# Optimization experiments

Hardware: AMD Instinct MI355X
Metric: run time of the kernel (lower is better)

Reference implementation:

```python
import jax, jax.numpy as jnp
from jax import lax
import numpy as np

LOD = 60          # latent_obs_dim
LSD = 2 * LOD     # latent state dim
ACT = 10          # action dim
K = 15            # num_basis
BW = 3            # bandwidth
H_CTRL = 60       # control net hidden units
B, T = 1024, 150


def elup1(x):
    # elu(x) + 1, standard RKN positive-variance activation
    return jnp.where(x >= 0, x + 1.0, jnp.exp(x))


def setup_inputs() -> dict:
    key = jax.random.key(0)
    ks = jax.random.split(key, 14)
    inp = {
        "latent_obs": jax.random.normal(ks[0], (B, T, LOD), jnp.float32),
        "obs_vars": jax.random.uniform(ks[1], (B, T, LOD), jnp.float32) + 0.01,
        "action": jax.random.normal(ks[2], (B, T, ACT), jnp.float32),
        "initial_mean": jax.random.normal(ks[3], (B, LSD), jnp.float32),
        "initial_cov_u": jnp.ones((B, LOD), jnp.float32),
        "initial_cov_l": jnp.ones((B, LOD), jnp.float32),
        "initial_cov_s": jnp.zeros((B, LOD), jnp.float32),
        # transition model: K banded basis matrices per quadrant
        "tm11_basis": 0.05 * jax.random.normal(ks[4], (K, LOD, LOD), jnp.float32),
        "tm12_basis": 0.05 * jax.random.normal(ks[5], (K, LOD, LOD), jnp.float32),
        "tm21_basis": 0.05 * jax.random.normal(ks[6], (K, LOD, LOD), jnp.float32),
        "tm22_basis": 0.05 * jax.random.normal(ks[7], (K, LOD, LOD), jnp.float32),
        # coefficient net: linear (no hidden units per default config) + softmax
        "coeff_w": 0.05 * jax.random.normal(ks[8], (LSD, K), jnp.float32),
        "coeff_b": jnp.zeros((K,), jnp.float32),
        # control net: act -> 60 -> ReLU -> lsd
        "ctrl_w1": (1.0 / np.sqrt(ACT)) * jax.random.normal(ks[9], (ACT, H_CTRL), jnp.float32),
        "ctrl_b1": jnp.zeros((H_CTRL,), jnp.float32),
        "ctrl_w2": (1.0 / np.sqrt(H_CTRL)) * jax.random.normal(ks[10], (H_CTRL, LSD), jnp.float32),
        "ctrl_b2": jnp.zeros((LSD,), jnp.float32),
        # learned transition noise (elup1(0) = 1 matches default trans_covar=1)
        "log_trans_cov": jnp.zeros((LSD,), jnp.float32),
    }
    return inp


def _band_mask():
    i = np.arange(LOD)
    return jnp.asarray((np.abs(i[:, None] - i[None, :]) <= BW).astype(np.float32))


def reference(latent_obs, obs_vars, action, initial_mean,
              initial_cov_u, initial_cov_l, initial_cov_s,
              tm11_basis, tm12_basis, tm21_basis, tm22_basis,
              coeff_w, coeff_b, ctrl_w1, ctrl_b1, ctrl_w2, ctrl_b2,
              log_trans_cov):
    mask = _band_mask()
    m11, m12 = tm11_basis * mask, tm12_basis * mask
    m21, m22 = tm21_basis * mask, tm22_basis * mask
    tc = elup1(log_trans_cov)
    tcu, tcl = tc[:LOD], tc[LOD:]

    def mv(tm, v):  # batched matrix-vector: [b,i,j] @ [b,j] -> [b,i]
        return jnp.einsum('bij,bj->bi', tm, v)

    def step(carry, xs):
        mean, cu, cl, cs = carry           # prior belief
        obs, ov, act = xs
        # ---- Update (factorized Kalman update) ----
        denom = cu + ov
        qu = cu / denom                    # upper Kalman gain
        ql = cs / denom                    # lower Kalman gain
        res = obs - mean[:, :LOD]
        post_mean = mean + jnp.concatenate([qu * res, ql * res], axis=-1)
        f = 1.0 - qu
        pcu = f * cu
        pcs = f * cs
        pcl = cl - ql * cs
        # ---- AcPredict (locally linear transition + control) ----
        coeff = jax.nn.softmax(post_mean @ coeff_w + coeff_b, axis=-1)  # [B,K]
        t11 = jnp.einsum('bk,kij->bij', coeff, m11)
        t12 = jnp.einsum('bk,kij->bij', coeff, m12)
        t21 = jnp.einsum('bk,kij->bij', coeff, m21)
        t22 = jnp.einsum('bk,kij->bij', coeff, m22)
        mu, ml = post_mean[:, :LOD], post_mean[:, LOD:]
        ctrl = jax.nn.relu(act @ ctrl_w1 + ctrl_b1) @ ctrl_w2 + ctrl_b2
        nmean = jnp.concatenate([mv(t11, mu) + mv(t12, ml),
                                 mv(t21, mu) + mv(t22, ml)], axis=-1) + ctrl
        # diag blocks of T C T^T with C block-diagonal (cu, cl, cs)
        ncu = mv(t11 ** 2, pcu) + 2.0 * mv(t11 * t12, pcs) + mv(t12 ** 2, pcl) + tcu
        ncl = mv(t21 ** 2, pcu) + 2.0 * mv(t21 * t22, pcs) + mv(t22 ** 2, pcl) + tcl
        ncs = mv(t21 * t11, pcu) + mv(t22 * t11 + t21 * t12, pcs) + mv(t22 * t12, pcl)
        out = (post_mean, pcu, pcl, pcs, nmean, ncu, ncl, ncs)
        return (nmean, ncu, ncl, ncs), out

    xs = (jnp.moveaxis(latent_obs, 1, 0),
          jnp.moveaxis(obs_vars, 1, 0),
          jnp.moveaxis(action, 1, 0))
    carry0 = (initial_mean, initial_cov_u, initial_cov_l, initial_cov_s)
    _, ys = lax.scan(step, carry0, xs)
    post_means, pcu, pcl, pcs, prior_means, ncu, ncl, ncs = [
        jnp.moveaxis(y, 0, 1) for y in ys]  # [B,T,...]
    return (post_means, pcu, pcl, pcs, prior_means, ncu, ncl, ncs)


if __name__ == "__main__":
    outs = reference(**setup_inputs())
    print([o.shape for o in outs])
```

## Files before the change

kernel.cpp:

```cpp
#include <hip/hip_runtime.h>
#include <hip/hip_bf16.h>

namespace {

constexpr int TT = 150;

__device__ __forceinline__ float dot4(float4 a, float4 b) {
  return a.x*b.x + a.y*b.y + a.z*b.z + a.w*b.w;
}
__device__ __forceinline__ unsigned short bf16bits(float v) {
  __hip_bfloat16 h = __float2bfloat16(v);
  return *reinterpret_cast<unsigned short*>(&h);
}
__device__ __forceinline__ float dot2bf(unsigned a, unsigned b, float c) {
  float d;
  asm("v_dot2_f32_bf16 %0, %1, %2, %3" : "=v"(d) : "v"(a), "v"(b), "v"(c));
  return d;
}
__device__ __forceinline__ float tdot(uint4 a, uint4 b, const unsigned* cp) {
  float s = 0.f;
  s = dot2bf(a.x, cp[0], s); s = dot2bf(a.y, cp[1], s);
  s = dot2bf(a.z, cp[2], s); s = dot2bf(a.w, cp[3], s);
  s = dot2bf(b.x, cp[4], s); s = dot2bf(b.y, cp[5], s);
  s = dot2bf(b.z, cp[6], s); s = dot2bf(b.w, cp[7], s);
  return s;
}

template<int D0, int ND>
__device__ __forceinline__ void tmv_part(const uint4* m4u, const unsigned* cepk,
                                         const float* stat, int ii, int b, int swz,
                                         float rv[5]) {
  #pragma unroll
  for (int dd = 0; dd < ND; ++dd) {
    const int d = D0 + dd;
    const int ba = (0*7 + d)*120 + ii*2;
    const int bb = (1*7 + d)*120 + ii*2;
    const int bc = (2*7 + d)*120 + ii*2;
    const int bd = (3*7 + d)*120 + ii*2;
    const uint4 xa = m4u[ba + swz], ya = m4u[ba + 1 - swz];
    const uint4 xb = m4u[bb + swz], yb = m4u[bb + 1 - swz];
    const uint4 xc = m4u[bc + swz], yc = m4u[bc + 1 - swz];
    const uint4 xd = m4u[bd + swz], yd = m4u[bd + 1 - swz];
    const float a11 = tdot(xa, ya, cepk);
    const float a12 = tdot(xb, yb, cepk);
    const float a21 = tdot(xc, yc, cepk);
    const float a22 = tdot(xd, yd, cepk);
    const int si = (ii + d)*4 + b;
    const float mun  = stat[si];
    const float mln  = stat[288  + si];
    const float pcun = stat[576  + si];
    const float pcsn = stat[864  + si];
    const float pcln = stat[1152 + si];
    rv[0] += a11*mun + a12*mln;
    rv[1] += a21*mun + a22*mln;
    rv[2] += a11*a11*pcun + 2.f*a11*a12*pcsn + a12*a12*pcln;
    rv[3] += a21*a21*pcun + 2.f*a21*a22*pcsn + a22*a22*pcln;
    rv[4] += a21*a11*pcun + (a22*a11 + a21*a12)*pcsn + a22*a12*pcln;
  }
}

__launch_bounds__(256, 4)
__global__ void ctrl_pre(const float* __restrict__ actp,
                         const float* __restrict__ w1,
                         const float* __restrict__ b1,
                         const float* __restrict__ w2,
                         const float* __restrict__ b2,
                         float* __restrict__ out)
{
  __shared__ float w1s[640];
  __shared__ float b1s[64];
  __shared__ __align__(16) float w2pk[7680];
  __shared__ float b2s[128];
  __shared__ __align__(16) float hbuf[256];

  const int tid = threadIdx.x;
  for (int idx = tid; idx < 640; idx += 256) {
    const int j = idx & 63, a = idx >> 6;
    w1s[idx] = (j < 60) ? w1[a*60 + j] : 0.f;
  }
  for (int idx = tid; idx < 7680; idx += 256) {
    const int e = idx & 3;
    const int l = (idx >> 2) & 63;
    const int rest = idx >> 8;
    const int j4 = rest % 15;
    const int p  = rest / 15;
    w2pk[idx] = (l < 60) ? w2[(4*j4 + e)*120 + 2*l + p] : 0.f;
  }
  if (tid < 64)  b1s[tid] = (tid < 60)  ? b1[tid] : 0.f;
  if (tid < 128) b2s[tid] = (tid < 120) ? b2[tid] : 0.f;
  __syncthreads();

  const int w = tid >> 6, lane = tid & 63;
  float* o4 = out + 46080000L;
  const float4* w2pk4 = (const float4*)w2pk;
  const float4* hb4   = (const float4*)hbuf;

  long bt = (long)(blockIdx.x*4 + w);
  float av = (lane < 10 && bt < 153600L) ? actp[bt*10 + lane] : 0.f;

  for (int it = 0; it < 10; ++it) {
    const long btn = bt + 16384L;
    const float avn = (lane < 10 && btn < 153600L) ? actp[btn*10 + lane] : 0.f;

    if (bt < 153600L) {
      float hj = b1s[lane];
      #pragma unroll
      for (int a = 0; a < 10; ++a) hj += __shfl(av, a) * w1s[a*64 + lane];
      hbuf[w*64 + lane] = (lane < 60) ? fmaxf(hj, 0.f) : 0.f;

      float s0 = 0.f, s1 = 0.f;
      if (lane < 60) { s0 = b2s[2*lane]; s1 = b2s[2*lane + 1]; }
      #pragma unroll
      for (int j4 = 0; j4 < 15; ++j4) {
        const float4 hq = hb4[w*16 + j4];
        s0 += dot4(hq, w2pk4[(0*15 + j4)*64 + lane]);
        s1 += dot4(hq, w2pk4[(1*15 + j4)*64 + lane]);
      }
      if (lane < 60) ((float2*)(o4 + bt*120))[lane] = make_float2(s0, s1);
    }
    bt = btn; av = avn;
  }
}

__launch_bounds__(1024, 4)
__global__ void acrkn(const float* __restrict__ lob,
                      const float* __restrict__ ovr,
                      const float* __restrict__ im,
                      const float* __restrict__ icu,
                      const float* __restrict__ icl,
                      const float* __restrict__ ics,
                      const float* __restrict__ tm11,
                      const float* __restrict__ tm12,
                      const float* __restrict__ tm21,
                      const float* __restrict__ tm22,
                      const float* __restrict__ cw,
                      const float* __restrict__ cb,
                      const float* __restrict__ ltc,
                      float* __restrict__ out)
{
  __shared__ __align__(16) unsigned m4b[13440];
  __shared__ __align__(16) float cwc[2048];
  __shared__ __align__(16) float stat[1440];
  __shared__ __align__(16) float pscratch[4096];
  __shared__ __align__(16) float parts[256];
  __shared__ __align__(16) float red[5120];
  __shared__ float cbs[16];

  const int tid = threadIdx.x;

  for (int idx = tid; idx < 13440; idx += 1024) {
    const int c2 = idx & 7;
    int rest = idx >> 3;
    const int i = rest % 60;  rest /= 60;
    const int d = rest % 7;
    const int mat = rest / 7;
    const int k0 = 2*c2;
    const int j = i + d - 3;
    const float* tp = (mat == 0) ? tm11 : (mat == 1) ? tm12 : (mat == 2) ? tm21 : tm22;
    float ve = 0.f, vo = 0.f;
    if (j >= 0 && j < 60) {
      ve = tp[(k0*60 + i)*60 + j];
      if (k0 + 1 < 15) vo = tp[((k0+1)*60 + i)*60 + j];
    }
    const unsigned u = ((unsigned)bf16bits(vo) << 16) | (unsigned)bf16bits(ve);
    const int s = c2 >> 2, q = c2 & 3;
    const int sp = s ^ ((i >> 2) & 1);
    m4b[(((mat*7 + d)*60 + i)*2 + sp)*4 + q] = u;
  }
  if (tid < 512) {
    const int f4 = tid;
    const int p = f4 & 127, c = f4 >> 7;
    const int col = (p < 60) ? p : ((p >= 64 && p < 124) ? (p - 4) : -1);
    float v0 = 0.f, v1 = 0.f, v2 = 0.f, v3 = 0.f;
    if (col >= 0) {
      const int k0 = c*4;
      v0 = cw[col*15 + k0+0];
      v1 = cw[col*15 + k0+1];
      v2 = cw[col*15 + k0+2];
      v3 = (k0+3 < 15) ? cw[col*15 + k0+3] : 0.f;
    }
    ((float4*)cwc)[f4] = make_float4(v0, v1, v2, v3);
  }
  for (int idx = tid; idx < 1440; idx += 1024) stat[idx] = 0.f;
  if (tid < 16) cbs[tid] = (tid < 15) ? cb[tid] : 0.f;

  const int w = tid >> 6;
  const int chunk = w >> 2;
  const int wq = w & 3;
  const int lane = tid & 63;
  const int r = lane >> 2;
  const int b = lane & 3;
  const int iraw = wq*16 + r;
  const bool valid = (iraw < 60);
  const int ii = valid ? iraw : 0;
  const int gb = blockIdx.x*4 + b;
  const int swz = (ii >> 2) & 1;

  float mu_c = 0.f, ml_c = 0.f, cu_c = 1.f, cl_c = 1.f, cs_c = 0.f;
  float tcu_r = 1.f, tcl_r = 1.f;
  if (valid) {
    mu_c = im[gb*120 + ii];
    ml_c = im[gb*120 + 60 + ii];
    cu_c = icu[gb*60 + ii];
    cl_c = icl[gb*60 + ii];
    cs_c = ics[gb*60 + ii];
    const float l0 = ltc[ii], l1 = ltc[60 + ii];
    tcu_r = (l0 >= 0.f) ? l0 + 1.f : __expf(l0);
    tcl_r = (l1 >= 0.f) ? l1 + 1.f : __expf(l1);
  }

  const uint4*  m4u    = (const uint4*)m4b;
  const float4* cwc4   = (const float4*)cwc;
  const float4* parts4 = (const float4*)parts;
  float4*       ps4    = (float4*)pscratch;

  float* o0 = out;
  float* o1 = out + 18432000L;
  float* o2 = out + 27648000L;
  float* o3 = out + 36864000L;
  float* o4 = out + 46080000L;
  float* o5 = out + 64512000L;
  float* o6 = out + 73728000L;
  float* o7 = out + 82944000L;

  __syncthreads();

  for (int t = 0; t < TT; ++t) {
    const long ob120 = ((long)gb*TT + t)*120;

    float ctrl_u = 0.f, ctrl_l = 0.f;
    if ((chunk == 0 || chunk == 3) && valid) {
      ctrl_u = o4[ob120 + ii];
      ctrl_l = o4[ob120 + 60 + ii];
    }

    if (chunk == 0) {
      const long ib = (long)gb*(TT*60) + t*60 + ii;
      float obs = 0.f, ovv = 1.f;
      if (valid) { obs = lob[ib]; ovv = ovr[ib]; }
      const float denom = cu_c + ovv;
      const float inv = 1.0f / denom;
      const float qu = cu_c * inv;
      const float ql = cs_c * inv;
      const float res = obs - mu_c;
      float pm_u = mu_c + qu*res;
      float pm_l = ml_c + ql*res;
      const float f1 = 1.f - qu;
      float pcu = f1*cu_c, pcs = f1*cs_c, pcl = cl_c - ql*cs_c;
      if (!valid) { pm_u = 0.f; pm_l = 0.f; pcu = 0.f; pcs = 0.f; pcl = 0.f; }

      if (valid) {
        stat[(0*72 + ii + 3)*4 + b] = pm_u;
        stat[(1*72 + ii + 3)*4 + b] = pm_l;
        stat[(2*72 + ii + 3)*4 + b] = pcu;
        stat[(3*72 + ii + 3)*4 + b] = pcs;
        stat[(4*72 + ii + 3)*4 + b] = pcl;
      }

      float p[16];
      #pragma unroll
      for (int k = 0; k < 16; ++k) p[k] = 0.f;
      #pragma unroll
      for (int c = 0; c < 4; ++c) {
        const float4 wu = cwc4[c*128 + ii];
        const float4 wl = cwc4[c*128 + 64 + ii];
        p[c*4+0] += pm_u*wu.x + pm_l*wl.x;
        p[c*4+1] += pm_u*wu.y + pm_l*wl.y;
        p[c*4+2] += pm_u*wu.z + pm_l*wl.z;
        p[c*4+3] += pm_u*wu.w + pm_l*wl.w;
      }
      const int pb = (wq*64 + lane)*4;
      ps4[pb+0] = make_float4(p[0],  p[1],  p[2],  p[3]);
      ps4[pb+1] = make_float4(p[4],  p[5],  p[6],  p[7]);
      ps4[pb+2] = make_float4(p[8],  p[9],  p[10], p[11]);
      ps4[pb+3] = make_float4(p[12], p[13], p[14], p[15]);
      const int rbase = wq*1024 + b*16 + r;
      float tv[16];
      #pragma unroll
      for (int rp = 0; rp < 16; ++rp) tv[rp] = pscratch[rbase + rp*64];
      const float s0 = (tv[0]+tv[1]) + (tv[2]+tv[3]);
      const float s1 = (tv[4]+tv[5]) + (tv[6]+tv[7]);
      const float s2 = (tv[8]+tv[9]) + (tv[10]+tv[11]);
      const float s3 = (tv[12]+tv[13]) + (tv[14]+tv[15]);
      parts[(wq*4 + b)*16 + r] = (s0+s1) + (s2+s3);
    }
    __syncthreads();

    if (chunk == 3 && valid) {
      const long ob60 = ((long)gb*TT + t)*60;
      const float s_pmu = stat[(0*72 + ii + 3)*4 + b];
      const float s_pml = stat[(1*72 + ii + 3)*4 + b];
      const float s_pcu = stat[(2*72 + ii + 3)*4 + b];
      const float s_pcs = stat[(3*72 + ii + 3)*4 + b];
      const float s_pcl = stat[(4*72 + ii + 3)*4 + b];
      o0[ob120 + ii]      = s_pmu;
      o0[ob120 + 60 + ii] = s_pml;
      o1[ob60 + ii] = s_pcu;
      o2[ob60 + ii] = s_pcl;
      o3[ob60 + ii] = s_pcs;
    }

    float q[16];
    #pragma unroll
    for (int k = 0; k < 16; ++k) q[k] = cbs[k];
    #pragma unroll
    for (int ww = 0; ww < 4; ++ww) {
      #pragma unroll
      for (int c = 0; c < 4; ++c) {
        const float4 pv = parts4[(ww*4 + b)*4 + c];
        q[4*c+0] += pv.x; q[4*c+1] += pv.y; q[4*c+2] += pv.z; q[4*c+3] += pv.w;
      }
    }
    float ce[16];
    #pragma unroll
    for (int k = 0; k < 15; ++k) ce[k] = __expf(q[k]);
    const float e0 = (ce[0]+ce[1]) + (ce[2]+ce[3]);
    const float e1 = (ce[4]+ce[5]) + (ce[6]+ce[7]);
    const float e2 = (ce[8]+ce[9]) + (ce[10]+ce[11]);
    const float e3 = (ce[12]+ce[13]) + ce[14];
    const float rs = 1.f / ((e0+e1) + (e2+e3));
    #pragma unroll
    for (int k = 0; k < 15; ++k) ce[k] *= rs;
    ce[15] = 0.f;
    unsigned cepk[8];
    #pragma unroll
    for (int j = 0; j < 8; ++j)
      cepk[j] = ((unsigned)bf16bits(ce[2*j+1]) << 16) | (unsigned)bf16bits(ce[2*j]);

    float rv[5] = {0.f, 0.f, 0.f, 0.f, 0.f};
    if      (chunk == 0) tmv_part<0, 2>(m4u, cepk, stat, ii, b, swz, rv);
    else if (chunk == 1) tmv_part<2, 2>(m4u, cepk, stat, ii, b, swz, rv);
    else if (chunk == 2) tmv_part<4, 2>(m4u, cepk, stat, ii, b, swz, rv);
    else                 tmv_part<6, 1>(m4u, cepk, stat, ii, b, swz, rv);

    if (valid) {
      #pragma unroll
      for (int v = 0; v < 5; ++v) red[chunk*1280 + v*256 + ii*4 + b] = rv[v];
    }
    __syncthreads();

    if (chunk == 0 || chunk == 3) {
      const int rb = ii*4 + b;
      float nmu = ctrl_u, nml = ctrl_l, ncu = tcu_r, ncl = tcl_r, ncs = 0.f;
      #pragma unroll
      for (int c = 0; c < 4; ++c) {
        nmu += red[c*1280 + 0*256 + rb];
        nml += red[c*1280 + 1*256 + rb];
        ncu += red[c*1280 + 2*256 + rb];
        ncl += red[c*1280 + 3*256 + rb];
        ncs += red[c*1280 + 4*256 + rb];
      }
      if (chunk == 3) {
        if (valid) {
          const long ob60 = ((long)gb*TT + t)*60;
          o4[ob120 + ii]      = nmu;
          o4[ob120 + 60 + ii] = nml;
          o5[ob60 + ii] = ncu;
          o6[ob60 + ii] = ncl;
          o7[ob60 + ii] = ncs;
        }
      } else {
        mu_c = nmu; ml_c = nml; cu_c = ncu; cl_c = ncl; cs_c = ncs;
      }
    }
  }
}

}

extern "C" void kernel_launch(void* const* d_in, const int* in_sizes, int n_in,
                              void* d_out, int out_size, void* d_ws, size_t ws_size,
                              hipStream_t stream) {
  (void)in_sizes; (void)n_in; (void)d_ws; (void)ws_size; (void)out_size;
  const float* lob  = (const float*)d_in[0];
  const float* ovr  = (const float*)d_in[1];
  const float* actp = (const float*)d_in[2];
  const float* im   = (const float*)d_in[3];
  const float* icu  = (const float*)d_in[4];
  const float* icl  = (const float*)d_in[5];
  const float* ics  = (const float*)d_in[6];
  const float* tm11 = (const float*)d_in[7];
  const float* tm12 = (const float*)d_in[8];
  const float* tm21 = (const float*)d_in[9];
  const float* tm22 = (const float*)d_in[10];
  const float* cw   = (const float*)d_in[11];
  const float* cb   = (const float*)d_in[12];
  const float* w1   = (const float*)d_in[13];
  const float* b1   = (const float*)d_in[14];
  const float* w2   = (const float*)d_in[15];
  const float* b2   = (const float*)d_in[16];
  const float* ltc  = (const float*)d_in[17];

  ctrl_pre<<<dim3(4096), dim3(256), 0, stream>>>(actp, w1, b1, w2, b2, (float*)d_out);
  acrkn<<<dim3(256), dim3(1024), 0, stream>>>(
      lob, ovr, im, icu, icl, ics,
      tm11, tm12, tm21, tm22, cw, cb, ltc,
      (float*)d_out);
}
```

Measured before the change: 725.2 us.

## Fuse control net into recurrent kernel using idle wave groups

Removes the separate ctrl_pre kernel and computes the control MLP per timestep inside the main scan kernel on chunks 1 and 2, which were idle during the update phase. The result goes into a double-buffered shared array instead of a global round trip through the prior-mean output. The pscratch reduction layout is also padded (stride 20) to reduce LDS bank conflicts. This adds shared memory (w2T, hctl, ctl) and per-step work on the critical path, which may lower occupancy or lengthen each step.

After: 627.5 us. 13.5% less time.

```diff
diff --git a/kernel.cpp b/kernel.cpp
--- a/kernel.cpp
+++ b/kernel.cpp
@@ -59,72 +59,10 @@
   }
 }
 
-__launch_bounds__(256, 4)
-__global__ void ctrl_pre(const float* __restrict__ actp,
-                         const float* __restrict__ w1,
-                         const float* __restrict__ b1,
-                         const float* __restrict__ w2,
-                         const float* __restrict__ b2,
-                         float* __restrict__ out)
-{
-  __shared__ float w1s[640];
-  __shared__ float b1s[64];
-  __shared__ __align__(16) float w2pk[7680];
-  __shared__ float b2s[128];
-  __shared__ __align__(16) float hbuf[256];
-
-  const int tid = threadIdx.x;
-  for (int idx = tid; idx < 640; idx += 256) {
-    const int j = idx & 63, a = idx >> 6;
-    w1s[idx] = (j < 60) ? w1[a*60 + j] : 0.f;
-  }
-  for (int idx = tid; idx < 7680; idx += 256) {
-    const int e = idx & 3;
-    const int l = (idx >> 2) & 63;
-    const int rest = idx >> 8;
-    const int j4 = rest % 15;
-    const int p  = rest / 15;
-    w2pk[idx] = (l < 60) ? w2[(4*j4 + e)*120 + 2*l + p] : 0.f;
-  }
-  if (tid < 64)  b1s[tid] = (tid < 60)  ? b1[tid] : 0.f;
-  if (tid < 128) b2s[tid] = (tid < 120) ? b2[tid] : 0.f;
-  __syncthreads();
-
-  const int w = tid >> 6, lane = tid & 63;
-  float* o4 = out + 46080000L;
-  const float4* w2pk4 = (const float4*)w2pk;
-  const float4* hb4   = (const float4*)hbuf;
-
-  long bt = (long)(blockIdx.x*4 + w);
-  float av = (lane < 10 && bt < 153600L) ? actp[bt*10 + lane] : 0.f;
-
-  for (int it = 0; it < 10; ++it) {
-    const long btn = bt + 16384L;
-    const float avn = (lane < 10 && btn < 153600L) ? actp[btn*10 + lane] : 0.f;
-
-    if (bt < 153600L) {
-      float hj = b1s[lane];
-      #pragma unroll
-      for (int a = 0; a < 10; ++a) hj += __shfl(av, a) * w1s[a*64 + lane];
-      hbuf[w*64 + lane] = (lane < 60) ? fmaxf(hj, 0.f) : 0.f;
-
-      float s0 = 0.f, s1 = 0.f;
-      if (lane < 60) { s0 = b2s[2*lane]; s1 = b2s[2*lane + 1]; }
-      #pragma unroll
-      for (int j4 = 0; j4 < 15; ++j4) {
-        const float4 hq = hb4[w*16 + j4];
-        s0 += dot4(hq, w2pk4[(0*15 + j4)*64 + lane]);
-        s1 += dot4(hq, w2pk4[(1*15 + j4)*64 + lane]);
-      }
-      if (lane < 60) ((float2*)(o4 + bt*120))[lane] = make_float2(s0, s1);
-    }
-    bt = btn; av = avn;
-  }
-}
-
 __launch_bounds__(1024, 4)
 __global__ void acrkn(const float* __restrict__ lob,
                       const float* __restrict__ ovr,
+                      const float* __restrict__ actp,
                       const float* __restrict__ im,
                       const float* __restrict__ icu,
                       const float* __restrict__ icl,
@@ -135,15 +73,25 @@
                       const float* __restrict__ tm22,
                       const float* __restrict__ cw,
                       const float* __restrict__ cb,
+                      const float* __restrict__ w1,
+                      const float* __restrict__ b1,
+                      const float* __restrict__ w2,
+                      const float* __restrict__ b2,
                       const float* __restrict__ ltc,
                       float* __restrict__ out)
 {
   __shared__ __align__(16) unsigned m4b[13440];
   __shared__ __align__(16) float cwc[2048];
   __shared__ __align__(16) float stat[1440];
-  __shared__ __align__(16) float pscratch[4096];
+  __shared__ __align__(16) float pscratch[5120];
   __shared__ __align__(16) float parts[256];
   __shared__ __align__(16) float red[5120];
+  __shared__ __align__(16) float ctl[1024];
+  __shared__ __align__(16) float hctl[512];
+  __shared__ __align__(16) float w2T[7680];
+  __shared__ float w1s[640];
+  __shared__ float b1s[64];
+  __shared__ float b2s[128];
   __shared__ float cbs[16];
 
   const int tid = threadIdx.x;
@@ -181,8 +129,22 @@
     }
     ((float4*)cwc)[f4] = make_float4(v0, v1, v2, v3);
   }
+  for (int idx = tid; idx < 7680; idx += 1024) {
+    const int e = idx & 3;
+    const int f4 = idx >> 2;
+    const int j4 = f4 % 15;
+    const int col = f4 / 15;
+    const int j = 4*j4 + e;
+    w2T[idx] = (j < 60 && col < 120) ? w2[j*120 + col] : 0.f;
+  }
+  for (int idx = tid; idx < 640; idx += 1024) {
+    const int j = idx & 63, a = idx >> 6;
+    w1s[idx] = (j < 60) ? w1[a*60 + j] : 0.f;
+  }
   for (int idx = tid; idx < 1440; idx += 1024) stat[idx] = 0.f;
-  if (tid < 16) cbs[tid] = (tid < 15) ? cb[tid] : 0.f;
+  if (tid < 64)  b1s[tid] = (tid < 60)  ? b1[tid] : 0.f;
+  if (tid < 128) b2s[tid] = (tid < 120) ? b2[tid] : 0.f;
+  if (tid < 16)  cbs[tid] = (tid < 15)  ? cb[tid] : 0.f;
 
   const int w = tid >> 6;
   const int chunk = w >> 2;
@@ -227,12 +189,6 @@
 
   for (int t = 0; t < TT; ++t) {
     const long ob120 = ((long)gb*TT + t)*120;
-
-    float ctrl_u = 0.f, ctrl_l = 0.f;
-    if ((chunk == 0 || chunk == 3) && valid) {
-      ctrl_u = o4[ob120 + ii];
-      ctrl_l = o4[ob120 + 60 + ii];
-    }
 
     if (chunk == 0) {
       const long ib = (long)gb*(TT*60) + t*60 + ii;
@@ -269,20 +225,34 @@
         p[c*4+2] += pm_u*wu.z + pm_l*wl.z;
         p[c*4+3] += pm_u*wu.w + pm_l*wl.w;
       }
-      const int pb = (wq*64 + lane)*4;
+      const int pb = (wq*64 + lane)*5;
       ps4[pb+0] = make_float4(p[0],  p[1],  p[2],  p[3]);
       ps4[pb+1] = make_float4(p[4],  p[5],  p[6],  p[7]);
       ps4[pb+2] = make_float4(p[8],  p[9],  p[10], p[11]);
       ps4[pb+3] = make_float4(p[12], p[13], p[14], p[15]);
-      const int rbase = wq*1024 + b*16 + r;
       float tv[16];
       #pragma unroll
-      for (int rp = 0; rp < 16; ++rp) tv[rp] = pscratch[rbase + rp*64];
+      for (int rp = 0; rp < 16; ++rp) tv[rp] = pscratch[(wq*64 + 4*rp + b)*20 + r];
       const float s0 = (tv[0]+tv[1]) + (tv[2]+tv[3]);
       const float s1 = (tv[4]+tv[5]) + (tv[6]+tv[7]);
       const float s2 = (tv[8]+tv[9]) + (tv[10]+tv[11]);
       const float s3 = (tv[12]+tv[13]) + (tv[14]+tv[15]);
       parts[(wq*4 + b)*16 + r] = (s0+s1) + (s2+s3);
+    } else if (chunk == 1 || chunk == 2) {
+      const int gbc = blockIdx.x*4 + wq;
+      const float av = (lane < 10) ? actp[((long)gbc*TT + t)*10 + lane] : 0.f;
+      float hj = b1s[lane];
+      #pragma unroll
+      for (int a = 0; a < 10; ++a) hj += __shfl(av, a) * w1s[a*64 + lane];
+      const int hw = w - 4;
+      hctl[hw*64 + lane] = (lane < 60) ? fmaxf(hj, 0.f) : 0.f;
+      const int col = (chunk == 1) ? lane : 60 + lane;
+      float s = (lane < 60) ? b2s[col] : 0.f;
+      const float4* hb4c = (const float4*)&hctl[hw*64];
+      #pragma unroll
+      for (int j4 = 0; j4 < 15; ++j4)
+        s += dot4(hb4c[j4], *(const float4*)&w2T[col*60 + j4*4]);
+      if (lane < 60) ctl[(t&1)*512 + wq*128 + col] = s;
     }
     __syncthreads();
 
@@ -340,6 +310,8 @@
     __syncthreads();
 
     if (chunk == 0 || chunk == 3) {
+      const float ctrl_u = ctl[(t&1)*512 + b*128 + ii];
+      const float ctrl_l = ctl[(t&1)*512 + b*128 + 60 + ii];
       const int rb = ii*4 + b;
       float nmu = ctrl_u, nml = ctrl_l, ncu = tcu_r, ncl = tcl_r, ncs = 0.f;
       #pragma unroll
@@ -391,9 +363,8 @@
   const float* b2   = (const float*)d_in[16];
   const float* ltc  = (const float*)d_in[17];
 
-  ctrl_pre<<<dim3(4096), dim3(256), 0, stream>>>(actp, w1, b1, w2, b2, (float*)d_out);
   acrkn<<<dim3(256), dim3(1024), 0, stream>>>(
-      lob, ovr, im, icu, icl, ics,
-      tm11, tm12, tm21, tm22, cw, cb, ltc,
+      lob, ovr, actp, im, icu, icl, ics,
+      tm11, tm12, tm21, tm22, cw, cb, w1, b1, w2, b2, ltc,
       (float*)d_out);
 }
```
